# Kernel tuning notes

Measured on AMD Instinct MI355X. Metric: run time of the kernel, lower is better.

Reference implementation:

```python
import jax, jax.numpy as jnp
import numpy as np

TIMESTEPS = 32
MAX_LATENCY = 31  # defaults to timesteps - 1


def setup_inputs() -> dict:
    key = jax.random.key(0)
    x = jax.random.uniform(key, (32, 3, 224, 224), dtype=jnp.float32)
    return {"x": x}


def reference(x):
    # Latency coding: first-spike time encodes magnitude.
    x_norm = jnp.clip(x, 0.0, 1.0)                                   # [B, ...]
    lat = ((1.0 - x_norm) * MAX_LATENCY).astype(jnp.int32)
    lat = jnp.clip(lat, 0, TIMESTEPS - 1)                            # [B, ...]
    # One-hot scatter along new time axis (axis=1), gated by x_norm > 0.
    t = jnp.arange(TIMESTEPS, dtype=jnp.int32).reshape(
        (1, TIMESTEPS) + (1,) * (x.ndim - 1))                        # [1, T, 1...]
    spikes = ((lat[:, None] == t) & (x_norm[:, None] > 0)).astype(jnp.float32)
    return spikes  # [B, T, ...]
```

## Files before the change

kernel.cpp:

```cpp
#include <hip/hip_runtime.h>

#define TIMESTEPS 32

__global__ __launch_bounds__(256) void LatencyCoding_kernel(
    const float* __restrict__ x, float* __restrict__ out,
    int n4, int spatial ) {

    int idx4 = blockIdx.x * blockDim.x + threadIdx.x;
    if (idx4 >= n4) return;

    float4 v = reinterpret_cast<const float4*>(x)[idx4];

    int elem = idx4 << 2;
    int b    = elem / spatial;
    int s    = elem - b * spatial;

    float comp[4] = {v.x, v.y, v.z, v.w};
    int   lat[4];
    bool  on[4];
#pragma unroll
    for (int j = 0; j < 4; ++j) {
        float xn = fminf(fmaxf(comp[j], 0.0f), 1.0f);
        int l = (int)((1.0f - xn) * 31.0f);
        l = min(max(l, 0), TIMESTEPS - 1);
        lat[j] = l;
        on[j]  = (xn > 0.0f);
    }

    float4* out4 = reinterpret_cast<float4*>(out + (size_t)b * TIMESTEPS * spatial + s);
    size_t stride4 = (size_t)(spatial >> 2);

#pragma unroll
    for (int t = 0; t < TIMESTEPS; ++t) {
        float4 o;
        o.x = (on[0] && lat[0] == t) ? 1.0f : 0.0f;
        o.y = (on[1] && lat[1] == t) ? 1.0f : 0.0f;
        o.z = (on[2] && lat[2] == t) ? 1.0f : 0.0f;
        o.w = (on[3] && lat[3] == t) ? 1.0f : 0.0f;
        out4[(size_t)t * stride4] = o;
    }
}

extern "C" void kernel_launch(void* const* d_in, const int* in_sizes, int n_in,
                              void* d_out, int out_size, void* d_ws, size_t ws_size,
                              hipStream_t stream) {
    const float* x  = (const float*)d_in[0];
    float*       out = (float*)d_out;

    int n = in_sizes[0];
    int spatial = n / 32;
    int n4 = n / 4;

    const int block = 256;
    int grid = (n4 + block - 1) / block;
    LatencyCoding_kernel<<<grid, block, 0, stream>>>(x, out, n4, spatial);
}
```

Before: 121.9 us.

## Parallelize over output planes with 2D grid, recomputing latency per timestep

```diff
diff --git a/kernel.cpp b/kernel.cpp
--- a/kernel.cpp
+++ b/kernel.cpp
@@ -1,57 +1,55 @@
 #include <hip/hip_runtime.h>
 
 #define TIMESTEPS 32
+#define UNROLL 4
 
 __global__ __launch_bounds__(256) void LatencyCoding_kernel(
-    const float* __restrict__ x, float* __restrict__ out,
-    int n4, int spatial ) {
+    const float* __restrict__ x, float* __restrict__ out, int spatial4) {
 
-    int idx4 = blockIdx.x * blockDim.x + threadIdx.x;
-    if (idx4 >= n4) return;
+    int plane = blockIdx.y;
+    int t = plane & (TIMESTEPS - 1);
+    int b = plane >> 5;
 
-    float4 v = reinterpret_cast<const float4*>(x)[idx4];
+    int s4_base = blockIdx.x * (256 * UNROLL) + threadIdx.x;
 
-    int elem = idx4 << 2;
-    int b    = elem / spatial;
-    int s    = elem - b * spatial;
-
-    float comp[4] = {v.x, v.y, v.z, v.w};
-    int   lat[4];
-    bool  on[4];
-#pragma unroll
-    for (int j = 0; j < 4; ++j) {
-        float xn = fminf(fmaxf(comp[j], 0.0f), 1.0f);
-        int l = (int)((1.0f - xn) * 31.0f);
-        l = min(max(l, 0), TIMESTEPS - 1);
-        lat[j] = l;
-        on[j]  = (xn > 0.0f);
-    }
-
-    float4* out4 = reinterpret_cast<float4*>(out + (size_t)b * TIMESTEPS * spatial + s);
-    size_t stride4 = (size_t)(spatial >> 2);
+    const float4* in4  = reinterpret_cast<const float4*>(x)   + (size_t)b     * spatial4;
+    float4*       out4 = reinterpret_cast<float4*>(out)       + (size_t)plane * spatial4;
 
 #pragma unroll
-    for (int t = 0; t < TIMESTEPS; ++t) {
-        float4 o;
-        o.x = (on[0] && lat[0] == t) ? 1.0f : 0.0f;
-        o.y = (on[1] && lat[1] == t) ? 1.0f : 0.0f;
-        o.z = (on[2] && lat[2] == t) ? 1.0f : 0.0f;
-        o.w = (on[3] && lat[3] == t) ? 1.0f : 0.0f;
-        out4[(size_t)t * stride4] = o;
+    for (int i = 0; i < UNROLL; ++i) {
+        int s4 = s4_base + i * 256;
+        if (s4 < spatial4) {
+            float4 v = in4[s4];
+            float c[4] = {v.x, v.y, v.z, v.w};
+            float r[4];
+#pragma unroll
+            for (int j = 0; j < 4; ++j) {
+                float xn = fminf(fmaxf(c[j], 0.0f), 1.0f);
+                int l = (int)((1.0f - xn) * 31.0f);
+                l = min(max(l, 0), TIMESTEPS - 1);
+                r[j] = (l == t && xn > 0.0f) ? 1.0f : 0.0f;
+            }
+            float4 o;
+            o.x = r[0]; o.y = r[1]; o.z = r[2]; o.w = r[3];
+            out4[s4] = o;
+        }
     }
 }
 
 extern "C" void kernel_launch(void* const* d_in, const int* in_sizes, int n_in,
                               void* d_out, int out_size, void* d_ws, size_t ws_size,
                               hipStream_t stream) {
-    const float* x  = (const float*)d_in[0];
+    const float* x   = (const float*)d_in[0];
     float*       out = (float*)d_out;
 
     int n = in_sizes[0];
-    int spatial = n / 32;
-    int n4 = n / 4;
+    int B = 32;
+    int spatial  = n / B;
+    int spatial4 = spatial / 4;
 
-    const int block = 256;
-    int grid = (n4 + block - 1) / block;
-    LatencyCoding_kernel<<<grid, block, 0, stream>>>(x, out, n4, spatial);
+    dim3 block(256, 1, 1);
+    int gx = (spatial4 + 256 * UNROLL - 1) / (256 * UNROLL);
+    dim3 grid(gx, B * TIMESTEPS, 1);
+
+    LatencyCoding_kernel<<<grid, block, 0, stream>>>(x, out, spatial4);
 }
```

New measurement: 172.3 us. 1.41x slower.
